# Kernel tuning notes

Hardware: AMD Instinct MI355X
Metric: run time of the kernel (lower is better)

The kernel has to match this reference:

```python
import jax, jax.numpy as jnp
import numpy as np

NUM_CAPSULE = 10
DIM_CAPSULE = 16
ROUTINGS = 3
EPS = 1e-7  # K.epsilon()


def squash(x, axis=-1):
    # bojone squash: x / sqrt(s2 + eps) * s2 / (1 + s2)
    s2 = jnp.sum(jnp.square(x), axis=axis, keepdims=True)
    return x * s2 / ((1.0 + s2) * jnp.sqrt(s2 + EPS))


def setup_inputs() -> dict:
    key = jax.random.key(0)
    k1, k2 = jax.random.split(key)
    B, N, D_in = 64, 2048, 128  # batch, input_num_capsule, input_dim_capsule
    u_vecs = jax.random.normal(k1, (B, N, D_in), dtype=jnp.float32)
    fan_out = NUM_CAPSULE * DIM_CAPSULE
    limit = float(np.sqrt(6.0 / (D_in + fan_out)))  # glorot_uniform
    W = jax.random.uniform(k2, (D_in, fan_out), dtype=jnp.float32,
                           minval=-limit, maxval=limit)
    return {"u_vecs": u_vecs, "W": W}


def reference(u_vecs, W):
    B, N, _ = u_vecs.shape
    # share_weights=True: conv1d with kernel size 1 == matmul over feature dim
    u_hat = (u_vecs @ W).reshape(B, N, NUM_CAPSULE, DIM_CAPSULE)
    u_hat = jnp.transpose(u_hat, (0, 2, 1, 3))  # (B, J, N, D)
    b = jnp.zeros((B, NUM_CAPSULE, N), dtype=u_vecs.dtype)
    o = jnp.zeros((B, NUM_CAPSULE, DIM_CAPSULE), dtype=u_vecs.dtype)
    for i in range(ROUTINGS):
        c = jax.nn.softmax(b, axis=1)           # softmax over output capsules
        o = jnp.einsum('bjn,bjnd->bjd', c, u_hat)
        if i < ROUTINGS - 1:
            b = jnp.einsum('bjd,bjnd->bjn', o, u_hat)  # agreement update
    return squash(o)
```

## Files before the change

### kernel.cpp

```cpp
#include <hip/hip_runtime.h>
#include <math.h>


#define BATCH 64
#define NN    2048
#define KD    128
#define JCAP  10
#define DCAP  16
#define JDIM  160
#define EPSQ  1e-7f
#define TPB   256

#define WS_SP   0
#define WS_V    65536
#define WS_GP1  147456
#define WS_O2P  802816

__global__ __launch_bounds__(TPB) void f_colsum(const float* __restrict__ u,
                                                float* __restrict__ Sp) {
  const int b = blockIdx.y, tile = blockIdx.x, t = threadIdx.x;
  const int k4 = (t & 31) * 4, rg = t >> 5;
  __shared__ float4 red[256];
  const float* p = u + ((size_t)(b * NN) + tile * 256 + rg * 32) * KD + k4;
  float4 a = make_float4(0.f, 0.f, 0.f, 0.f);
#pragma unroll 4
  for (int r = 0; r < 32; ++r) {
    float4 w = *(const float4*)(p + (size_t)r * KD);
    a.x += w.x; a.y += w.y; a.z += w.z; a.w += w.w;
  }
  red[t] = a;
  __syncthreads();
  if (t < 32) {
    float4 s4 = red[t];
#pragma unroll
    for (int rg2 = 1; rg2 < 8; ++rg2) {
      float4 w = red[rg2 * 32 + t];
      s4.x += w.x; s4.y += w.y; s4.z += w.z; s4.w += w.w;
    }
    *(float4*)&Sp[(size_t)(b * 8 + tile) * KD + t * 4] = s4;
  }
}

__global__ __launch_bounds__(TPB) void f_makeV(const float* __restrict__ ws,
                                               const float* __restrict__ W,
                                               float* __restrict__ V,
                                               int pass) {
  const int b = blockIdx.x, t = threadIdx.x;
  __shared__ float gsum[JCAP * KD];
  __shared__ float o_s[JDIM];
  if (pass == 0) {
    const float* Sp = ws + WS_SP + (size_t)b * 8 * KD;
    if (t < KD) {
      float s = 0.f;
#pragma unroll
      for (int tl = 0; tl < 8; ++tl) s += Sp[tl * KD + t];
      gsum[t] = s * 0.1f;
    }
  } else {
    const float* Gp1 = ws + WS_GP1 + (size_t)b * 8 * JCAP * KD;
    for (int i = t; i < JCAP * KD; i += TPB) {
      float s = 0.f;
#pragma unroll
      for (int tl = 0; tl < 8; ++tl) s += Gp1[tl * JCAP * KD + i];
      gsum[i] = s;
    }
  }
  __syncthreads();
  if (t < JDIM) {
    const int j = t >> 4;
    const float* gs = pass == 0 ? gsum : (gsum + j * KD);
    float acc = 0.f;
#pragma unroll 4
    for (int k = 0; k < KD; ++k) acc += gs[k] * W[k * JDIM + t];
    o_s[t] = acc;
  }
  __syncthreads();
  const int k = t & 127, gg = t >> 7;
#pragma unroll
  for (int i = 0; i < 5; ++i) {
    const int j = gg * 5 + i;
    const float* wp = W + k * JDIM + j * DCAP;
    float acc = 0.f;
#pragma unroll
    for (int d = 0; d < DCAP; ++d) acc += wp[d] * o_s[j * DCAP + d];
    V[(size_t)(b * JCAP + j) * KD + k] = acc;
  }
}

__global__ __launch_bounds__(TPB) void f_route(const float* __restrict__ u,
                                               const float* __restrict__ V,
                                               const float* __restrict__ W,
                                               float* __restrict__ dst,
                                               int pass) {
  const int b = blockIdx.y, tile = blockIdx.x, t = threadIdx.x;
  const int r0 = tile * 256;
  __shared__ __align__(16) float Cs[JCAP][260];
  __shared__ __align__(16) float Gp[4][JCAP][KD];
  {
    const float* up = u + (size_t)(b * NN + r0 + t) * KD;
    const float* vb = V + (size_t)(b * JCAP) * KD;
    float acc[JCAP];
#pragma unroll
    for (int j = 0; j < JCAP; ++j) acc[j] = 0.f;
    for (int kc = 0; kc < KD; kc += 8) {
      float4 xa = *(const float4*)(up + kc);
      float4 xb = *(const float4*)(up + kc + 4);
#pragma unroll
      for (int j = 0; j < JCAP; ++j) {
        float4 v0 = *(const float4*)(vb + j * KD + kc);
        float4 v1 = *(const float4*)(vb + j * KD + kc + 4);
        acc[j] += xa.x * v0.x + xa.y * v0.y + xa.z * v0.z + xa.w * v0.w
                + xb.x * v1.x + xb.y * v1.y + xb.z * v1.z + xb.w * v1.w;
      }
    }
    float m = acc[0];
#pragma unroll
    for (int j = 1; j < JCAP; ++j) m = fmaxf(m, acc[j]);
    float s = 0.f;
#pragma unroll
    for (int j = 0; j < JCAP; ++j) { acc[j] = __expf(acc[j] - m); s += acc[j]; }
    const float inv = 1.f / s;
#pragma unroll
    for (int j = 0; j < JCAP; ++j) Cs[j][t] = acc[j] * inv;
  }
  __syncthreads();
  {
    const int wave = t >> 6, lane = t & 63;
    const int rw = wave * 64;
    float g0[JCAP], g1[JCAP];
#pragma unroll
    for (int j = 0; j < JCAP; ++j) { g0[j] = 0.f; g1[j] = 0.f; }
    const float* ub = u + (size_t)(b * NN + r0 + rw) * KD + 2 * lane;
    for (int rc = 0; rc < 64; rc += 4) {
      float ua[4], uc[4];
#pragma unroll
      for (int q = 0; q < 4; ++q) {
        float2 w = *(const float2*)(ub + (size_t)(rc + q) * KD);
        ua[q] = w.x; uc[q] = w.y;
      }
#pragma unroll
      for (int j = 0; j < JCAP; ++j) {
        float4 c4 = *(const float4*)&Cs[j][rw + rc];
        g0[j] += c4.x * ua[0] + c4.y * ua[1] + c4.z * ua[2] + c4.w * ua[3];
        g1[j] += c4.x * uc[0] + c4.y * uc[1] + c4.z * uc[2] + c4.w * uc[3];
      }
    }
#pragma unroll
    for (int j = 0; j < JCAP; ++j)
      *(float2*)&Gp[wave][j][2 * lane] = make_float2(g0[j], g1[j]);
  }
  __syncthreads();
  if (pass == 0) {
    float* Gp1 = dst + (size_t)(b * 8 + tile) * JCAP * KD;
    for (int i = t; i < JCAP * KD; i += TPB)
      Gp1[i] = Gp[0][0][i] + Gp[1][0][i] + Gp[2][0][i] + Gp[3][0][i];
  } else {
    for (int i = t; i < JCAP * KD; i += TPB)
      Gp[0][0][i] = Gp[0][0][i] + Gp[1][0][i] + Gp[2][0][i] + Gp[3][0][i];
    __syncthreads();
    if (t < JDIM) {
      const int j = t >> 4;
      float acc = 0.f;
#pragma unroll 4
      for (int k = 0; k < KD; ++k) acc += Gp[0][j][k] * W[k * JDIM + t];
      dst[(size_t)(b * 8 + tile) * JDIM + t] = acc;
    }
  }
}

__global__ __launch_bounds__(TPB) void f_squash(const float* __restrict__ O2p,
                                                float* __restrict__ out) {
  const int b = blockIdx.x, t = threadIdx.x;
  __shared__ float o_s[JDIM];
  __shared__ float sc[JCAP];
  if (t < JDIM) {
    const float* p = O2p + (size_t)b * 8 * JDIM;
    float s = 0.f;
#pragma unroll
    for (int tl = 0; tl < 8; ++tl) s += p[tl * JDIM + t];
    o_s[t] = s;
  }
  __syncthreads();
  if (t < JCAP) {
    float s2 = 0.f;
#pragma unroll
    for (int d = 0; d < DCAP; ++d) { float x = o_s[t * DCAP + d]; s2 += x * x; }
    sc[t] = s2 / ((1.f + s2) * sqrtf(s2 + EPSQ));
  }
  __syncthreads();
  if (t < JDIM) out[b * JDIM + t] = o_s[t] * sc[t >> 4];
}

extern "C" void kernel_launch(void* const* d_in, const int* in_sizes, int n_in,
                              void* d_out, int out_size, void* d_ws, size_t ws_size,
                              hipStream_t stream) {
  const float* u = (const float*)d_in[0];
  const float* W = (const float*)d_in[1];
  float* out = (float*)d_out;
  float* ws  = (float*)d_ws;

  float* Sp  = ws + WS_SP;
  float* V   = ws + WS_V;
  float* Gp1 = ws + WS_GP1;
  float* O2p = ws + WS_O2P;
  f_colsum<<<dim3(8, BATCH), TPB, 0, stream>>>(u, Sp);
  f_makeV <<<BATCH, TPB, 0, stream>>>(ws, W, V, 0);
  f_route <<<dim3(8, BATCH), TPB, 0, stream>>>(u, V, W, Gp1, 0);
  f_makeV <<<BATCH, TPB, 0, stream>>>(ws, W, V, 1);
  f_route <<<dim3(8, BATCH), TPB, 0, stream>>>(u, V, W, O2p, 1);
  f_squash<<<BATCH, TPB, 0, stream>>>(O2p, out);
}
```

Measured before the change: 172.5 us.

## Restage routing through LDS with smaller tiles and per-tile projected partials

Routing tiles shrink from 256 to 64 rows, giving 2048 blocks instead of 512. Each block copies its u tile once into XOR-swizzled LDS using global_load_lds, and both the logit dot products and the weighted sum then read from LDS instead of re-reading global memory. Every pass, iteration 0 included, now projects its partial sum through W inside the block and writes a 160-wide partial. makeV is split across (capsule, batch) blocks, and the separate colsum kernel is folded into iter0. The cost is more partial sums to reduce, 32 per batch instead of 8, and more W traffic per block.

```diff
diff --git a/kernel.cpp b/kernel.cpp
--- a/kernel.cpp
+++ b/kernel.cpp
@@ -9,182 +9,197 @@
 #define DCAP  16
 #define JDIM  160
 #define EPSQ  1e-7f
-#define TPB   256
-
-#define WS_SP   0
-#define WS_V    65536
-#define WS_GP1  147456
-#define WS_O2P  802816
-
-__global__ __launch_bounds__(TPB) void f_colsum(const float* __restrict__ u,
-                                                float* __restrict__ Sp) {
+#define NT    32
+#define TROW  64
+
+#define WS_OP 0
+#define WS_V  (BATCH * NT * JDIM)
+
+__device__ __forceinline__ void gload16(const float* g, float4* l) {
+  __builtin_amdgcn_global_load_lds(
+      (const __attribute__((address_space(1))) void*)g,
+      (__attribute__((address_space(3))) void*)l, 16, 0, 0);
+}
+
+__global__ __launch_bounds__(256) void f_iter0(const float* __restrict__ u,
+                                               const float* __restrict__ W,
+                                               float* __restrict__ Op) {
   const int b = blockIdx.y, tile = blockIdx.x, t = threadIdx.x;
-  const int k4 = (t & 31) * 4, rg = t >> 5;
-  __shared__ float4 red[256];
-  const float* p = u + ((size_t)(b * NN) + tile * 256 + rg * 32) * KD + k4;
+  __shared__ __align__(16) float4 red[256];
+  __shared__ float S_s[KD];
+  const int c = t & 31, rg = t >> 5;
+  const float* p = u + (((size_t)(b * NN + tile * TROW + rg * 8)) << 7) + (c << 2);
   float4 a = make_float4(0.f, 0.f, 0.f, 0.f);
-#pragma unroll 4
-  for (int r = 0; r < 32; ++r) {
-    float4 w = *(const float4*)(p + (size_t)r * KD);
-    a.x += w.x; a.y += w.y; a.z += w.z; a.w += w.w;
+#pragma unroll
+  for (int r = 0; r < 8; ++r) {
+    const float4 w4 = *(const float4*)(p + ((size_t)r << 7));
+    a.x += w4.x; a.y += w4.y; a.z += w4.z; a.w += w4.w;
   }
   red[t] = a;
   __syncthreads();
   if (t < 32) {
     float4 s4 = red[t];
 #pragma unroll
-    for (int rg2 = 1; rg2 < 8; ++rg2) {
-      float4 w = red[rg2 * 32 + t];
-      s4.x += w.x; s4.y += w.y; s4.z += w.z; s4.w += w.w;
-    }
-    *(float4*)&Sp[(size_t)(b * 8 + tile) * KD + t * 4] = s4;
-  }
-}
-
-__global__ __launch_bounds__(TPB) void f_makeV(const float* __restrict__ ws,
+    for (int g = 1; g < 8; ++g) {
+      const float4 w4 = red[g * 32 + t];
+      s4.x += w4.x; s4.y += w4.y; s4.z += w4.z; s4.w += w4.w;
+    }
+    s4.x *= 0.1f; s4.y *= 0.1f; s4.z *= 0.1f; s4.w *= 0.1f;
+    *(float4*)&S_s[t * 4] = s4;
+  }
+  __syncthreads();
+  if (t < JDIM) {
+    float acc = 0.f;
+#pragma unroll 4
+    for (int k = 0; k < KD; ++k) acc += S_s[k] * W[k * JDIM + t];
+    Op[((size_t)(b * NT) + tile) * JDIM + t] = acc;
+  }
+}
+
+__global__ __launch_bounds__(128) void f_makeV(const float* __restrict__ Op,
                                                const float* __restrict__ W,
-                                               float* __restrict__ V,
-                                               int pass) {
-  const int b = blockIdx.x, t = threadIdx.x;
-  __shared__ float gsum[JCAP * KD];
-  __shared__ float o_s[JDIM];
-  if (pass == 0) {
-    const float* Sp = ws + WS_SP + (size_t)b * 8 * KD;
-    if (t < KD) {
-      float s = 0.f;
-#pragma unroll
-      for (int tl = 0; tl < 8; ++tl) s += Sp[tl * KD + t];
-      gsum[t] = s * 0.1f;
-    }
-  } else {
-    const float* Gp1 = ws + WS_GP1 + (size_t)b * 8 * JCAP * KD;
-    for (int i = t; i < JCAP * KD; i += TPB) {
-      float s = 0.f;
-#pragma unroll
-      for (int tl = 0; tl < 8; ++tl) s += Gp1[tl * JCAP * KD + i];
-      gsum[i] = s;
-    }
-  }
+                                               float* __restrict__ V) {
+  const int j = blockIdx.x, b = blockIdx.y, t = threadIdx.x;
+  __shared__ float o_s[DCAP];
+  if (t < DCAP) {
+    float s = 0.f;
+    const float* p = Op + (size_t)b * NT * JDIM + j * DCAP + t;
+#pragma unroll
+    for (int tl = 0; tl < NT; ++tl) s += p[tl * JDIM];
+    o_s[t] = s;
+  }
+  __syncthreads();
+  const float* wp = W + t * JDIM + j * DCAP;
+  float acc = 0.f;
+#pragma unroll
+  for (int d = 0; d < DCAP; ++d) acc += wp[d] * o_s[d];
+  V[((size_t)(b * JCAP + j) << 7) + t] = acc;
+}
+
+__global__ __launch_bounds__(256) void f_route(const float* __restrict__ u,
+                                               const float* __restrict__ V,
+                                               const float* __restrict__ W,
+                                               float* __restrict__ Op) {
+  const int b = blockIdx.y, tile = blockIdx.x, t = threadIdx.x;
+  const int r0 = tile * TROW;
+  __shared__ __align__(16) float4 u4[TROW * 32];
+  __shared__ __align__(16) float Cs[JCAP][TROW];
+  __shared__ __align__(16) float Gp[4 * JCAP * KD];
+
+  {
+    const float* ub = u + (((size_t)(b * NN + r0)) << 7);
+    const int wbase = t & 192;
+#pragma unroll
+    for (int p = 0; p < 8; ++p) {
+      const int s = p * 256 + t;
+      const int r = s >> 5, csl = s & 31;
+      const int c = csl ^ (r & 7);
+      gload16(ub + (((size_t)r) << 7) + (c << 2), &u4[p * 256 + wbase]);
+    }
+  }
+  __syncthreads();
+
+  {
+    const int r = t & 63;
+    const int q = __builtin_amdgcn_readfirstlane(t >> 6);
+    const float* vb = V + (((size_t)(b * JCAP)) << 7) + (q << 5);
+    float acc[JCAP];
+#pragma unroll
+    for (int j = 0; j < JCAP; ++j) acc[j] = 0.f;
+#pragma unroll
+    for (int c4 = 0; c4 < 8; ++c4) {
+      const float4 uu = u4[(r << 5) + ((q * 8 + c4) ^ (r & 7))];
+#pragma unroll
+      for (int j = 0; j < JCAP; ++j) {
+        const float4 vv = *(const float4*)(vb + (j << 7) + (c4 << 2));
+        acc[j] += uu.x * vv.x + uu.y * vv.y + uu.z * vv.z + uu.w * vv.w;
+      }
+    }
+    float* Pl = Gp;
+#pragma unroll
+    for (int j = 0; j < JCAP; ++j) Pl[(q * JCAP + j) * 64 + r] = acc[j];
+  }
+  __syncthreads();
+  if (t < TROW) {
+    const float* Pl = Gp;
+    float lg[JCAP];
+    float m = -1e30f;
+#pragma unroll
+    for (int j = 0; j < JCAP; ++j) {
+      const float s = Pl[j * 64 + t] + Pl[(JCAP + j) * 64 + t]
+                    + Pl[(2 * JCAP + j) * 64 + t] + Pl[(3 * JCAP + j) * 64 + t];
+      lg[j] = s; m = fmaxf(m, s);
+    }
+    float ssum = 0.f;
+#pragma unroll
+    for (int j = 0; j < JCAP; ++j) { lg[j] = __expf(lg[j] - m); ssum += lg[j]; }
+    const float inv = 1.f / ssum;
+#pragma unroll
+    for (int j = 0; j < JCAP; ++j) Cs[j][t] = lg[j] * inv;
+  }
+  __syncthreads();
+
+  {
+    const int w = t >> 6, lane = t & 63;
+    const int rw = w * 16;
+    const int chalf = lane >> 1, cin = (lane & 1) << 1;
+    float g0[JCAP], g1[JCAP];
+#pragma unroll
+    for (int j = 0; j < JCAP; ++j) { g0[j] = 0.f; g1[j] = 0.f; }
+    for (int rc = 0; rc < 16; rc += 4) {
+      float ua[4], uc[4];
+#pragma unroll
+      for (int qq = 0; qq < 4; ++qq) {
+        const int r = rw + rc + qq;
+        const float2 uu2 =
+            *(const float2*)((const float*)&u4[(r << 5) + (chalf ^ (r & 7))] + cin);
+        ua[qq] = uu2.x; uc[qq] = uu2.y;
+      }
+#pragma unroll
+      for (int j = 0; j < JCAP; ++j) {
+        const float4 c4v = *(const float4*)&Cs[j][rw + rc];
+        g0[j] += c4v.x * ua[0] + c4v.y * ua[1] + c4v.z * ua[2] + c4v.w * ua[3];
+        g1[j] += c4v.x * uc[0] + c4v.y * uc[1] + c4v.z * uc[2] + c4v.w * uc[3];
+      }
+    }
+#pragma unroll
+    for (int j = 0; j < JCAP; ++j)
+      *(float2*)&Gp[(w * JCAP + j) * KD + 2 * lane] = make_float2(g0[j], g1[j]);
+  }
+  __syncthreads();
+  for (int i = t; i < JCAP * KD; i += 256)
+    Gp[i] += Gp[JCAP * KD + i] + Gp[2 * JCAP * KD + i] + Gp[3 * JCAP * KD + i];
   __syncthreads();
   if (t < JDIM) {
     const int j = t >> 4;
-    const float* gs = pass == 0 ? gsum : (gsum + j * KD);
+    const float* gj = Gp + j * KD;
     float acc = 0.f;
 #pragma unroll 4
-    for (int k = 0; k < KD; ++k) acc += gs[k] * W[k * JDIM + t];
-    o_s[t] = acc;
-  }
-  __syncthreads();
-  const int k = t & 127, gg = t >> 7;
-#pragma unroll
-  for (int i = 0; i < 5; ++i) {
-    const int j = gg * 5 + i;
-    const float* wp = W + k * JDIM + j * DCAP;
-    float acc = 0.f;
-#pragma unroll
-    for (int d = 0; d < DCAP; ++d) acc += wp[d] * o_s[j * DCAP + d];
-    V[(size_t)(b * JCAP + j) * KD + k] = acc;
-  }
-}
-
-__global__ __launch_bounds__(TPB) void f_route(const float* __restrict__ u,
-                                               const float* __restrict__ V,
-                                               const float* __restrict__ W,
-                                               float* __restrict__ dst,
-                                               int pass) {
-  const int b = blockIdx.y, tile = blockIdx.x, t = threadIdx.x;
-  const int r0 = tile * 256;
-  __shared__ __align__(16) float Cs[JCAP][260];
-  __shared__ __align__(16) float Gp[4][JCAP][KD];
-  {
-    const float* up = u + (size_t)(b * NN + r0 + t) * KD;
-    const float* vb = V + (size_t)(b * JCAP) * KD;
-    float acc[JCAP];
-#pragma unroll
-    for (int j = 0; j < JCAP; ++j) acc[j] = 0.f;
-    for (int kc = 0; kc < KD; kc += 8) {
-      float4 xa = *(const float4*)(up + kc);
-      float4 xb = *(const float4*)(up + kc + 4);
-#pragma unroll
-      for (int j = 0; j < JCAP; ++j) {
-        float4 v0 = *(const float4*)(vb + j * KD + kc);
-        float4 v1 = *(const float4*)(vb + j * KD + kc + 4);
-        acc[j] += xa.x * v0.x + xa.y * v0.y + xa.z * v0.z + xa.w * v0.w
-                + xb.x * v1.x + xb.y * v1.y + xb.z * v1.z + xb.w * v1.w;
-      }
-    }
-    float m = acc[0];
-#pragma unroll
-    for (int j = 1; j < JCAP; ++j) m = fmaxf(m, acc[j]);
-    float s = 0.f;
-#pragma unroll
-    for (int j = 0; j < JCAP; ++j) { acc[j] = __expf(acc[j] - m); s += acc[j]; }
-    const float inv = 1.f / s;
-#pragma unroll
-    for (int j = 0; j < JCAP; ++j) Cs[j][t] = acc[j] * inv;
-  }
-  __syncthreads();
-  {
-    const int wave = t >> 6, lane = t & 63;
-    const int rw = wave * 64;
-    float g0[JCAP], g1[JCAP];
-#pragma unroll
-    for (int j = 0; j < JCAP; ++j) { g0[j] = 0.f; g1[j] = 0.f; }
-    const float* ub = u + (size_t)(b * NN + r0 + rw) * KD + 2 * lane;
-    for (int rc = 0; rc < 64; rc += 4) {
-      float ua[4], uc[4];
-#pragma unroll
-      for (int q = 0; q < 4; ++q) {
-        float2 w = *(const float2*)(ub + (size_t)(rc + q) * KD);
-        ua[q] = w.x; uc[q] = w.y;
-      }
-#pragma unroll
-      for (int j = 0; j < JCAP; ++j) {
-        float4 c4 = *(const float4*)&Cs[j][rw + rc];
-        g0[j] += c4.x * ua[0] + c4.y * ua[1] + c4.z * ua[2] + c4.w * ua[3];
-        g1[j] += c4.x * uc[0] + c4.y * uc[1] + c4.z * uc[2] + c4.w * uc[3];
-      }
-    }
-#pragma unroll
-    for (int j = 0; j < JCAP; ++j)
-      *(float2*)&Gp[wave][j][2 * lane] = make_float2(g0[j], g1[j]);
-  }
-  __syncthreads();
-  if (pass == 0) {
-    float* Gp1 = dst + (size_t)(b * 8 + tile) * JCAP * KD;
-    for (int i = t; i < JCAP * KD; i += TPB)
-      Gp1[i] = Gp[0][0][i] + Gp[1][0][i] + Gp[2][0][i] + Gp[3][0][i];
-  } else {
-    for (int i = t; i < JCAP * KD; i += TPB)
-      Gp[0][0][i] = Gp[0][0][i] + Gp[1][0][i] + Gp[2][0][i] + Gp[3][0][i];
-    __syncthreads();
-    if (t < JDIM) {
-      const int j = t >> 4;
-      float acc = 0.f;
-#pragma unroll 4
-      for (int k = 0; k < KD; ++k) acc += Gp[0][j][k] * W[k * JDIM + t];
-      dst[(size_t)(b * 8 + tile) * JDIM + t] = acc;
-    }
-  }
-}
-
-__global__ __launch_bounds__(TPB) void f_squash(const float* __restrict__ O2p,
+    for (int kk = 0; kk < KD; ++kk) {
+      const int k = (kk + 3 * j) & 127;
+      acc += gj[k] * W[k * JDIM + t];
+    }
+    Op[((size_t)(b * NT) + tile) * JDIM + t] = acc;
+  }
+}
+
+__global__ __launch_bounds__(192) void f_squash(const float* __restrict__ Op,
                                                 float* __restrict__ out) {
   const int b = blockIdx.x, t = threadIdx.x;
   __shared__ float o_s[JDIM];
   __shared__ float sc[JCAP];
   if (t < JDIM) {
-    const float* p = O2p + (size_t)b * 8 * JDIM;
     float s = 0.f;
-#pragma unroll
-    for (int tl = 0; tl < 8; ++tl) s += p[tl * JDIM + t];
+    const float* p = Op + (size_t)b * NT * JDIM + t;
+#pragma unroll
+    for (int tl = 0; tl < NT; ++tl) s += p[tl * JDIM];
     o_s[t] = s;
   }
   __syncthreads();
   if (t < JCAP) {
     float s2 = 0.f;
 #pragma unroll
-    for (int d = 0; d < DCAP; ++d) { float x = o_s[t * DCAP + d]; s2 += x * x; }
+    for (int d = 0; d < DCAP; ++d) { const float x = o_s[t * DCAP + d]; s2 += x * x; }
     sc[t] = s2 / ((1.f + s2) * sqrtf(s2 + EPSQ));
   }
   __syncthreads();
@@ -199,14 +214,12 @@
   float* out = (float*)d_out;
   float* ws  = (float*)d_ws;
 
-  float* Sp  = ws + WS_SP;
-  float* V   = ws + WS_V;
-  float* Gp1 = ws + WS_GP1;
-  float* O2p = ws + WS_O2P;
-  f_colsum<<<dim3(8, BATCH), TPB, 0, stream>>>(u, Sp);
-  f_makeV <<<BATCH, TPB, 0, stream>>>(ws, W, V, 0);
-  f_route <<<dim3(8, BATCH), TPB, 0, stream>>>(u, V, W, Gp1, 0);
-  f_makeV <<<BATCH, TPB, 0, stream>>>(ws, W, V, 1);
-  f_route <<<dim3(8, BATCH), TPB, 0, stream>>>(u, V, W, O2p, 1);
-  f_squash<<<BATCH, TPB, 0, stream>>>(O2p, out);
-}
+  float* Op = ws + WS_OP;
+  float* V  = ws + WS_V;
+  f_iter0 <<<dim3(NT, BATCH), 256, 0, stream>>>(u, W, Op);
+  f_makeV <<<dim3(JCAP, BATCH), 128, 0, stream>>>(Op, W, V);
+  f_route <<<dim3(NT, BATCH), 256, 0, stream>>>(u, V, W, Op);
+  f_makeV <<<dim3(JCAP, BATCH), 128, 0, stream>>>(Op, W, V);
+  f_route <<<dim3(NT, BATCH), 256, 0, stream>>>(u, V, W, Op);
+  f_squash<<<BATCH, 192, 0, stream>>>(Op, out);
+}
```

Measured after the change: 201.7 us. 16.9% more time.
